# Kernel tuning notes

Hardware: AMD Instinct MI355X
Metric: run time of the kernel (lower is better)

The kernel has to match this reference:

```python
import jax, jax.numpy as jnp
import numpy as np

N, E, G = 20000, 50000, 64          # nodes, edges, graphs
IN_DIM, EDGE_DIM, H, OUT_DIM = 32, 16, 64, 6
EPS = 1e-5  # BatchNorm eps


def setup_inputs() -> dict:
    key = jax.random.key(0)
    ks = jax.random.split(key, 24)
    s = 0.05
    inp = {
        "x": jax.random.normal(ks[0], (N, IN_DIM), jnp.float32),
        "edge_attr": jax.random.normal(ks[1], (E, EDGE_DIM), jnp.float32),
        "src": jax.random.randint(ks[2], (E,), 0, N, jnp.int32),
        "dst": jax.random.randint(ks[3], (E,), 0, N, jnp.int32),
        "batch": jnp.sort(jax.random.randint(ks[4], (N,), 0, G, jnp.int32)),
        # node encoder
        "Wx": jax.random.normal(ks[5], (IN_DIM, H), jnp.float32) * s,
        "bx": jnp.zeros((H,), jnp.float32),
        # three edge MLPs: edge_dim -> H*H
        "We": jax.random.normal(ks[6], (3, EDGE_DIM, H * H), jnp.float32) * s,
        "be": jnp.zeros((3, H * H), jnp.float32),
        # NNConv root weights / biases
        "Wroot": jax.random.normal(ks[7], (3, H, H), jnp.float32) * s,
        "broot": jnp.zeros((3, H), jnp.float32),
        # BatchNorm (eval mode: running stats)
        "gamma": jnp.ones((3, H), jnp.float32),
        "beta": jnp.zeros((3, H), jnp.float32),
        "run_mean": jnp.zeros((3, H), jnp.float32),
        "run_var": jnp.ones((3, H), jnp.float32),
        # head
        "W1": jax.random.normal(ks[8], (H, H), jnp.float32) * s,
        "b1": jnp.zeros((H,), jnp.float32),
        "W2": jax.random.normal(ks[9], (H, OUT_DIM), jnp.float32) * s,
        "b2": jnp.zeros((OUT_DIM,), jnp.float32),
    }
    return inp


def _segment_mean(vals, idx, num_segments):
    tot = jax.ops.segment_sum(vals, idx, num_segments=num_segments)
    cnt = jax.ops.segment_sum(jnp.ones((vals.shape[0],), vals.dtype), idx,
                              num_segments=num_segments)
    return tot / jnp.maximum(cnt, 1.0)[:, None]


def reference(x, edge_attr, src, dst, batch, Wx, bx, We, be, Wroot, broot,
              gamma, beta, run_mean, run_var, W1, b1, W2, b2):
    h = x @ Wx + bx                                      # (N, H)
    for l in range(3):
        # per-edge H x H weight matrices from the edge MLP
        ew = jax.nn.relu(edge_attr @ We[l] + be[l]).reshape(-1, H, H)  # (E, H, H)
        msg = jnp.einsum('eh,eho->eo', h[src], ew)       # gather + per-edge matvec
        agg = _segment_mean(msg, dst, N)                 # scatter-mean at destinations
        out = agg + h @ Wroot[l] + broot[l]              # NNConv root + bias
        out = jax.nn.relu(out)
        # BatchNorm1d in eval mode (running stats); dropout is identity in eval
        out = gamma[l] * (out - run_mean[l]) * jax.lax.rsqrt(run_var[l] + EPS) + beta[l]
        h = out + h                                      # residual (shapes always match)
    pooled = _segment_mean(h, batch, G)                  # global_mean_pool -> (G, H)
    z = jax.nn.relu(pooled @ W1 + b1)
    return z @ W2 + b2                                   # (G, OUT_DIM)
```

## Files before the change

kernel.cpp:

```cpp
#include <hip/hip_runtime.h>
#include <hip/hip_bf16.h>

typedef _Float16 f16x2 __attribute__((ext_vector_type(2)));
typedef _Float16 f16x4 __attribute__((ext_vector_type(4)));
typedef _Float16 f16x8 __attribute__((ext_vector_type(8)));
typedef float    f32x4 __attribute__((ext_vector_type(4)));
typedef float    f32x16 __attribute__((ext_vector_type(16)));

#define IN_DIM   32
#define EDGE_DIM 16
#define HDIM     64
#define OUT_DIM  6
#define BN_EPS   1e-5f

__global__ void k_zero(uint4* __restrict__ p, int n16) {
    int i = blockIdx.x * 256 + threadIdx.x;
    if (i < n16) p[i] = make_uint4(0u, 0u, 0u, 0u);
}

__global__ __launch_bounds__(256) void k_setup(
    const float* __restrict__ We, uint4* __restrict__ WeB,
    const float* __restrict__ x, const float* __restrict__ Wx,
    const float* __restrict__ bx, float* __restrict__ h,
    const float* __restrict__ ea, _Float16* __restrict__ eaH,
    const int* __restrict__ dstI, int* __restrict__ degI,
    const int* __restrict__ batch, int* __restrict__ start,
    int N, int E, int G, int PACKB, int ENCB, int PREPB)
{
    int bid = blockIdx.x;
    int t = threadIdx.x;

    if (bid < PACKB) {
        int tid = bid * 256 + t;
        int tile = tid >> 6, lane = tid & 63;
        int layer = tile >> 7;
        int r = tile & 127;
        int hh = r >> 1, oh = r & 1;
        int col = hh * 64 + oh * 32 + (lane & 31);
        int kbase = 8 * (lane >> 5);
        const float* base = We + (size_t)layer * 65536 + col;
        f16x8 v;
        #pragma unroll
        for (int j = 0; j < 8; ++j) v[j] = (_Float16)base[(size_t)(kbase + j) * 4096];
        WeB[(size_t)tile * 64 + lane] = __builtin_bit_cast(uint4, v);
        return;
    }
    bid -= PACKB;
    if (bid < ENCB) {
        int tid = bid * 256 + t;
        int n = tid >> 4, jq = tid & 15;
        if (n >= N) return;
        const float4* W4 = (const float4*)Wx;
        float4 acc = ((const float4*)bx)[jq];
        const float4* xv = (const float4*)(x + (size_t)n * IN_DIM);
        #pragma unroll
        for (int k4 = 0; k4 < 8; ++k4) {
            float4 xk = xv[k4];
            #pragma unroll
            for (int i = 0; i < 4; ++i) {
                float xs = (i == 0) ? xk.x : (i == 1) ? xk.y : (i == 2) ? xk.z : xk.w;
                float4 ww = W4[(k4 * 4 + i) * 16 + jq];
                acc.x += xs * ww.x; acc.y += xs * ww.y; acc.z += xs * ww.z; acc.w += xs * ww.w;
            }
        }
        ((float4*)h)[tid] = acc;
        return;
    }
    bid -= ENCB;
    if (bid < PREPB) {
        int tid = bid * 256 + t;
        int E8 = E * 8;
        if (tid < E8) {
            float2 v = ((const float2*)ea)[tid];
            f16x2 r; r[0] = (_Float16)v.x; r[1] = (_Float16)v.y;
            ((f16x2*)eaH)[tid] = r;
        }
        if (tid < E) atomicAdd(&degI[dstI[tid]], 1);
        return;
    }
    if (t <= G) {
        int lo = 0, hi = N;
        while (lo < hi) { int mid = (lo + hi) >> 1; if (batch[mid] < t) lo = mid + 1; else hi = mid; }
        start[t] = lo;
    }
}

__global__ void k_scan_local(const int* __restrict__ degI, int* __restrict__ rowptr,
                             int* __restrict__ partials, int N) {
    __shared__ int buf[256];
    int b = blockIdx.x, t = threadIdx.x;
    int i = b * 256 + t;
    int v = (i < N) ? degI[i] : 0;
    buf[t] = v;
    __syncthreads();
    #pragma unroll
    for (int ofs = 1; ofs < 256; ofs <<= 1) {
        int xv = (t >= ofs) ? buf[t - ofs] : 0;
        __syncthreads();
        buf[t] += xv;
        __syncthreads();
    }
    if (i < N) rowptr[i] = buf[t] - v;
    if (t == 255) partials[b] = buf[255];
}

__global__ void k_scan_top(int* __restrict__ partials, int nb) {
    __shared__ int buf[256];
    int t = threadIdx.x;
    int v = (t < nb) ? partials[t] : 0;
    buf[t] = v;
    __syncthreads();
    #pragma unroll
    for (int ofs = 1; ofs < 256; ofs <<= 1) {
        int xv = (t >= ofs) ? buf[t - ofs] : 0;
        __syncthreads();
        buf[t] += xv;
        __syncthreads();
    }
    if (t < nb) partials[t] = buf[t] - v;
    if (t == 0) partials[nb] = buf[255];
}

__global__ void k_scan_add(int* __restrict__ rowptr, int* __restrict__ cursor,
                           const int* __restrict__ partials, int N, int nb) {
    int i = blockIdx.x * 256 + threadIdx.x;
    if (i < N) {
        int r = rowptr[i] + partials[blockIdx.x];
        rowptr[i] = r;
        cursor[i] = r;
    }
    if (i == 0) rowptr[N] = partials[nb];
}

__global__ void k_place(const int* __restrict__ dstI, int* __restrict__ cursor,
                        int* __restrict__ eidx, int E) {
    int e = blockIdx.x * 256 + threadIdx.x;
    if (e < E) {
        int p = atomicAdd(&cursor[dstI[e]], 1);
        eidx[p] = e;
    }
}

__global__ __launch_bounds__(256, 6) void k_edge(
    const uint4* __restrict__ eaH4,
    const uint4* __restrict__ WeB,
    const float* __restrict__ be,
    const float* __restrict__ hin,
    const int* __restrict__ srcI,
    _Float16* __restrict__ msgP,
    int E)
{
    __shared__ float hsT[32][68];
    __shared__ float beL[2048];
    const int t = threadIdx.x;
    const int l = t & 63;
    const int w = t >> 6;
    const int eg = blockIdx.x >> 1;
    const int hhalf = blockIdx.x & 1;
    const int eb = eg * 64;
    const int hbase = hhalf * 32;

    {
        int egc = min(eb + l, E - 1);
        int s = srcI[egc];
        const float4* hp = (const float4*)(hin + (size_t)s * HDIM + hbase + w * 8);
        float4 a = hp[0], b = hp[1];
        hsT[w*8+0][l] = a.x; hsT[w*8+1][l] = a.y; hsT[w*8+2][l] = a.z; hsT[w*8+3][l] = a.w;
        hsT[w*8+4][l] = b.x; hsT[w*8+5][l] = b.y; hsT[w*8+6][l] = b.z; hsT[w*8+7][l] = b.w;
    }
    {
        const float4* bg = (const float4*)(be + hbase * 64);
        float4* bs = (float4*)beL;
        bs[t] = bg[t];
        bs[256 + t] = bg[256 + t];
    }
    __syncthreads();

    const int gp  = w >> 1;
    const int oh  = w & 1;
    const int ebw = eb + gp * 32;
    const int elw = gp * 32;
    const int row = l & 31;
    const int kg  = l >> 5;
    const int obase = oh * 32;

    int ea_e = min(ebw + row, E - 1);
    f16x8 A = __builtin_bit_cast(f16x8, eaH4[(size_t)ea_e * 2 + kg]);

    float m[16];
    #pragma unroll
    for (int j = 0; j < 16; ++j) m[j] = 0.f;

    const uint4* Bb = WeB + (size_t)(hbase * 2 + oh) * 64 + l;
    uint4 Bv = Bb[0];

    for (int hh = 0; hh < 32; ++hh) {
        uint4 Bn;
        if (hh < 31) Bn = Bb[(size_t)(hh + 1) * 128];
        float bias = beL[hh * 64 + obase + (l & 31)];
        f32x16 cin;
        #pragma unroll
        for (int j = 0; j < 16; ++j) cin[j] = bias;
        f32x16 z = __builtin_amdgcn_mfma_f32_32x32x16_f16(
            A, __builtin_bit_cast(f16x8, Bv), cin, 0, 0, 0);
        float4 q0 = *(const float4*)&hsT[hh][elw + 4 * kg + 0];
        float4 q1 = *(const float4*)&hsT[hh][elw + 4 * kg + 8];
        float4 q2 = *(const float4*)&hsT[hh][elw + 4 * kg + 16];
        float4 q3 = *(const float4*)&hsT[hh][elw + 4 * kg + 24];
        m[0]  += fmaxf(z[0],  0.f) * q0.x;
        m[1]  += fmaxf(z[1],  0.f) * q0.y;
        m[2]  += fmaxf(z[2],  0.f) * q0.z;
        m[3]  += fmaxf(z[3],  0.f) * q0.w;
        m[4]  += fmaxf(z[4],  0.f) * q1.x;
        m[5]  += fmaxf(z[5],  0.f) * q1.y;
        m[6]  += fmaxf(z[6],  0.f) * q1.z;
        m[7]  += fmaxf(z[7],  0.f) * q1.w;
        m[8]  += fmaxf(z[8],  0.f) * q2.x;
        m[9]  += fmaxf(z[9],  0.f) * q2.y;
        m[10] += fmaxf(z[10], 0.f) * q2.z;
        m[11] += fmaxf(z[11], 0.f) * q2.w;
        m[12] += fmaxf(z[12], 0.f) * q3.x;
        m[13] += fmaxf(z[13], 0.f) * q3.y;
        m[14] += fmaxf(z[14], 0.f) * q3.z;
        m[15] += fmaxf(z[15], 0.f) * q3.w;
        Bv = Bn;
    }

    _Float16* mw = msgP + (size_t)hhalf * E * 64 + obase + (l & 31);
    #pragma unroll
    for (int j = 0; j < 16; ++j) {
        int e = ebw + (j & 3) + 8 * (j >> 2) + 4 * kg;
        if (e < E) mw[(size_t)e * 64] = (_Float16)m[j];
    }
}

__global__ void k_update(
    const _Float16* __restrict__ msgP, const int* __restrict__ rowptr,
    const int* __restrict__ eidx,
    const float* __restrict__ hin, const float* __restrict__ Wroot,
    const float* __restrict__ broot, const float* __restrict__ gam,
    const float* __restrict__ bet, const float* __restrict__ rmean,
    const float* __restrict__ rvar, float* __restrict__ hout, int N, int E)
{
    int tid = blockIdx.x * 256 + threadIdx.x;
    int n = tid >> 4, jq = tid & 15;
    if (n >= N) return;
    int r0 = rowptr[n], r1 = rowptr[n + 1];
    float4 s = make_float4(0.f, 0.f, 0.f, 0.f);
    const f16x4* m4 = (const f16x4*)msgP;
    for (int i = r0; i < r1; ++i) {
        int eid = eidx[i];
        f16x4 a = m4[(size_t)eid * 16 + jq];
        f16x4 b = m4[((size_t)E + eid) * 16 + jq];
        s.x += (float)a[0] + (float)b[0];
        s.y += (float)a[1] + (float)b[1];
        s.z += (float)a[2] + (float)b[2];
        s.w += (float)a[3] + (float)b[3];
    }
    float dinv = 1.0f / fmaxf((float)(r1 - r0), 1.0f);
    float4 acc = ((const float4*)broot)[jq];
    acc.x += s.x * dinv; acc.y += s.y * dinv; acc.z += s.z * dinv; acc.w += s.w * dinv;
    const float4* W4 = (const float4*)Wroot;
    const float4* hv = (const float4*)(hin + (size_t)n * HDIM);
    #pragma unroll
    for (int k4 = 0; k4 < 16; ++k4) {
        float4 hk = hv[k4];
        #pragma unroll
        for (int i = 0; i < 4; ++i) {
            float hsc = (i == 0) ? hk.x : (i == 1) ? hk.y : (i == 2) ? hk.z : hk.w;
            float4 ww = W4[(k4 * 4 + i) * 16 + jq];
            acc.x += hsc * ww.x; acc.y += hsc * ww.y; acc.z += hsc * ww.z; acc.w += hsc * ww.w;
        }
    }
    acc.x = fmaxf(acc.x, 0.f); acc.y = fmaxf(acc.y, 0.f);
    acc.z = fmaxf(acc.z, 0.f); acc.w = fmaxf(acc.w, 0.f);
    float4 g4 = ((const float4*)gam)[jq];
    float4 b4 = ((const float4*)bet)[jq];
    float4 mm4 = ((const float4*)rmean)[jq];
    float4 v4 = ((const float4*)rvar)[jq];
    float4 hres = ((const float4*)hin)[tid];
    float4 y;
    y.x = g4.x * (acc.x - mm4.x) * rsqrtf(v4.x + BN_EPS) + b4.x + hres.x;
    y.y = g4.y * (acc.y - mm4.y) * rsqrtf(v4.y + BN_EPS) + b4.y + hres.y;
    y.z = g4.z * (acc.z - mm4.z) * rsqrtf(v4.z + BN_EPS) + b4.z + hres.z;
    y.w = g4.w * (acc.w - mm4.w) * rsqrtf(v4.w + BN_EPS) + b4.w + hres.w;
    ((float4*)hout)[tid] = y;
}

__global__ __launch_bounds__(256) void k_pool_head(
    const float* __restrict__ h, const int* __restrict__ start,
    const float* __restrict__ W1, const float* __restrict__ b1,
    const float* __restrict__ W2, const float* __restrict__ b2,
    float* __restrict__ out)
{
    __shared__ float sums[16][68];
    __shared__ float pl[HDIM];
    __shared__ float zl[HDIM];
    int g = blockIdx.x;
    int s0 = start[g], s1 = start[g + 1];
    int t = threadIdx.x, jq = t & 15, rp = t >> 4;
    float4 acc = make_float4(0.f, 0.f, 0.f, 0.f);
    for (int n = s0 + rp; n < s1; n += 16) {
        float4 v = ((const float4*)h)[(size_t)n * 16 + jq];
        acc.x += v.x; acc.y += v.y; acc.z += v.z; acc.w += v.w;
    }
    *(float4*)&sums[rp][jq * 4] = acc;
    __syncthreads();
    if (t < HDIM) {
        float a = 0.f;
        #pragma unroll
        for (int r = 0; r < 16; ++r) a += sums[r][t];
        float cnt = (float)(s1 - s0);
        pl[t] = a / fmaxf(cnt, 1.0f);
    }
    __syncthreads();
    if (t < HDIM) {
        float a = b1[t];
        #pragma unroll
        for (int k = 0; k < HDIM; ++k) a += pl[k] * W1[k * HDIM + t];
        zl[t] = fmaxf(a, 0.f);
    }
    __syncthreads();
    if (t < OUT_DIM) {
        float a = b2[t];
        #pragma unroll
        for (int k = 0; k < HDIM; ++k) a += zl[k] * W2[k * OUT_DIM + t];
        out[(size_t)g * OUT_DIM + t] = a;
    }
}

extern "C" void kernel_launch(void* const* d_in, const int* in_sizes, int n_in,
                              void* d_out, int out_size, void* d_ws, size_t ws_size,
                              hipStream_t stream) {
    const float* x     = (const float*)d_in[0];
    const float* eattr = (const float*)d_in[1];
    const int*   src   = (const int*)d_in[2];
    const int*   dst   = (const int*)d_in[3];
    const int*   batch = (const int*)d_in[4];
    const float* Wx    = (const float*)d_in[5];
    const float* bx    = (const float*)d_in[6];
    const float* We    = (const float*)d_in[7];
    const float* be    = (const float*)d_in[8];
    const float* Wroot = (const float*)d_in[9];
    const float* broot = (const float*)d_in[10];
    const float* gam   = (const float*)d_in[11];
    const float* bet   = (const float*)d_in[12];
    const float* rmean = (const float*)d_in[13];
    const float* rvar  = (const float*)d_in[14];
    const float* W1    = (const float*)d_in[15];
    const float* b1    = (const float*)d_in[16];
    const float* W2    = (const float*)d_in[17];
    const float* b2    = (const float*)d_in[18];
    float* out = (float*)d_out;

    const int N = in_sizes[0] / IN_DIM;
    const int E = in_sizes[2];
    const int G = out_size / OUT_DIM;

    char* ws = (char*)d_ws;
    size_t off = 0;
    auto alloc = [&](size_t bytes) -> void* {
        void* p = ws + off;
        off = (off + bytes + 255) & ~(size_t)255;
        return p;
    };
    float*    h0      = (float*)alloc((size_t)N * HDIM * 4);
    float*    h1      = (float*)alloc((size_t)N * HDIM * 4);
    _Float16* eaH     = (_Float16*)alloc((size_t)E * 16 * 2);
    uint4*    WeB     = (uint4*)alloc((size_t)3 * 128 * 64 * 16);
    int*      start   = (int*)alloc((size_t)(G + 1) * 4);
    int*      rowptr  = (int*)alloc((size_t)(N + 1) * 4);
    int*      cursor  = (int*)alloc((size_t)N * 4);
    int*      eidx    = (int*)alloc((size_t)E * 4);
    _Float16* msgP    = (_Float16*)alloc((size_t)2 * E * HDIM * 2);
    int*      degI    = (int*)alloc((size_t)((N + 3) & ~3) * 4);
    const int nb      = (N + 255) / 256;
    int*      partials= (int*)alloc((size_t)(nb + 1) * 4);
    (void)ws_size; (void)n_in;

    const int n16 = ((N + 3) & ~3) / 4;
    k_zero<<<(n16 + 255) / 256, 256, 0, stream>>>((uint4*)degI, n16);

    const int PACKB = 96;
    const int ENCB  = (N * 16 + 255) / 256;
    const int PREPB = (E * 8 + 255) / 256;
    k_setup<<<PACKB + ENCB + PREPB + 1, 256, 0, stream>>>(
        We, WeB, x, Wx, bx, h0, eattr, eaH, dst, degI, batch, start,
        N, E, G, PACKB, ENCB, PREPB);
    k_scan_local<<<nb, 256, 0, stream>>>(degI, rowptr, partials, N);
    k_scan_top<<<1, 256, 0, stream>>>(partials, nb);
    k_scan_add<<<nb, 256, 0, stream>>>(rowptr, cursor, partials, N, nb);
    k_place<<<(E + 255) / 256, 256, 0, stream>>>(dst, cursor, eidx, E);

    const float* hin = h0;
    float* hout = h1;
    const int edgeBlocks = ((E + 63) / 64) * 2;
    for (int l = 0; l < 3; ++l) {
        k_edge<<<edgeBlocks, 256, 0, stream>>>(
            (const uint4*)eaH, WeB + (size_t)l * 8192, be + (size_t)l * 4096,
            hin, src, msgP, E);
        k_update<<<(N * 16 + 255) / 256, 256, 0, stream>>>(
            msgP, rowptr, eidx, hin, Wroot + (size_t)l * 4096, broot + (size_t)l * 64,
            gam + (size_t)l * 64, bet + (size_t)l * 64, rmean + (size_t)l * 64,
            rvar + (size_t)l * 64, hout, N, E);
        float* tmp = hout; hout = (float*)hin; hin = tmp;
    }
    k_pool_head<<<G, 256, 0, stream>>>(hin, start, W1, b1, W2, b2, out);
}
```

Measured before the change: 195.2 us.

## Fuse whole GNN pipeline into one cooperative kernel with atomic scatter aggregation

Replaces the multi-kernel pipeline (setup, CSR scan/place, per-layer edge and update kernels, pooling) with a single cooperative persistent kernel that uses grid-wide syncs between phases. The CSR build and fp16 message buffer are dropped: edge blocks now cover all 64 input channels and atomically add fp32 messages into a per-node aggregation buffer, which the update phase reads and clears. This removes kernel launch overhead, the scan kernels and a message round-trip through memory. In exchange it adds float atomics contention, grid-sync costs and possibly lower occupancy from the larger shared memory footprint, plus nondeterministic summation order.

```diff
diff --git a/kernel.cpp b/kernel.cpp
--- a/kernel.cpp
+++ b/kernel.cpp
@@ -1,5 +1,8 @@
 #include <hip/hip_runtime.h>
 #include <hip/hip_bf16.h>
+#include <hip/hip_cooperative_groups.h>
+
+namespace cg = cooperative_groups;
 
 typedef _Float16 f16x2 __attribute__((ext_vector_type(2)));
 typedef _Float16 f16x4 __attribute__((ext_vector_type(4)));
@@ -12,6 +15,268 @@
 #define HDIM     64
 #define OUT_DIM  6
 #define BN_EPS   1e-5f
+
+struct FusedParams {
+    const float *x, *ea, *We, *be, *Wx, *bx, *Wroot, *broot, *gam, *bet, *rmean, *rvar, *W1, *b1, *W2, *b2;
+    const int *src, *dst, *batch;
+    float *out;
+    float *h0, *h1, *agg;
+    _Float16 *eaH;
+    uint4 *WeB;
+    int *degI, *start;
+    int N, E, G;
+};
+
+__global__ __launch_bounds__(256, 4) void k_fused(FusedParams p) {
+    cg::grid_group grid = cg::this_grid();
+    __shared__ __align__(16) float hsT[64][68];
+    __shared__ float beL[4096];
+    const int t  = threadIdx.x;
+    const int l  = t & 63;
+    const int w  = t >> 6;
+    const int b0 = blockIdx.x;
+    const int gs = gridDim.x;
+
+    {
+        int nz = p.N * 16;
+        for (int i = b0 * 256 + t; i < nz; i += gs * 256)
+            ((uint4*)p.agg)[i] = make_uint4(0u, 0u, 0u, 0u);
+        for (int i = b0 * 256 + t; i < p.N; i += gs * 256) p.degI[i] = 0;
+    }
+    grid.sync();
+
+    {
+        const int PACKB = 96;
+        const int ENCB  = (p.N * 16 + 255) / 256;
+        const int PREPB = (p.E * 8 + 255) / 256;
+        const int VB    = PACKB + ENCB + PREPB + 1;
+        for (int vb = b0; vb < VB; vb += gs) {
+            if (vb < PACKB) {
+                int tid = vb * 256 + t;
+                int tile = tid >> 6, lane = tid & 63;
+                int layer = tile >> 7;
+                int r = tile & 127;
+                int hh = r >> 1, oh = r & 1;
+                int col = hh * 64 + oh * 32 + (lane & 31);
+                int kbase = 8 * (lane >> 5);
+                const float* base = p.We + (size_t)layer * 65536 + col;
+                f16x8 v;
+                #pragma unroll
+                for (int j = 0; j < 8; ++j) v[j] = (_Float16)base[(size_t)(kbase + j) * 4096];
+                p.WeB[(size_t)tile * 64 + lane] = __builtin_bit_cast(uint4, v);
+            } else if (vb < PACKB + ENCB) {
+                int tid = (vb - PACKB) * 256 + t;
+                int n = tid >> 4, jq = tid & 15;
+                if (n < p.N) {
+                    const float4* W4 = (const float4*)p.Wx;
+                    float4 acc = ((const float4*)p.bx)[jq];
+                    const float4* xv = (const float4*)(p.x + (size_t)n * IN_DIM);
+                    #pragma unroll
+                    for (int k4 = 0; k4 < 8; ++k4) {
+                        float4 xk = xv[k4];
+                        #pragma unroll
+                        for (int i = 0; i < 4; ++i) {
+                            float xs = (i == 0) ? xk.x : (i == 1) ? xk.y : (i == 2) ? xk.z : xk.w;
+                            float4 ww = W4[(k4 * 4 + i) * 16 + jq];
+                            acc.x += xs * ww.x; acc.y += xs * ww.y;
+                            acc.z += xs * ww.z; acc.w += xs * ww.w;
+                        }
+                    }
+                    ((float4*)p.h0)[tid] = acc;
+                }
+            } else if (vb < PACKB + ENCB + PREPB) {
+                int tid = (vb - PACKB - ENCB) * 256 + t;
+                int E8 = p.E * 8;
+                if (tid < E8) {
+                    float2 v = ((const float2*)p.ea)[tid];
+                    f16x2 r2; r2[0] = (_Float16)v.x; r2[1] = (_Float16)v.y;
+                    ((f16x2*)p.eaH)[tid] = r2;
+                }
+                if (tid < p.E) atomicAdd(&p.degI[p.dst[tid]], 1);
+            } else {
+                if (t <= p.G) {
+                    int lo = 0, hi = p.N;
+                    while (lo < hi) { int mid = (lo + hi) >> 1; if (p.batch[mid] < t) lo = mid + 1; else hi = mid; }
+                    p.start[t] = lo;
+                }
+            }
+        }
+    }
+    grid.sync();
+
+    const int EG  = (p.E + 63) / 64;
+    const int NBu = (p.N * 16 + 255) / 256;
+    float* ha = p.h0;
+    float* hb = p.h1;
+
+    #pragma unroll 1
+    for (int layer = 0; layer < 3; ++layer) {
+        const float* hin = ha;
+        float* hout = hb;
+        const uint4* WeL = p.WeB + (size_t)layer * 8192;
+        const float* beG = p.be + (size_t)layer * 4096;
+
+        {
+            const float4* bg = (const float4*)beG;
+            float4* bs = (float4*)beL;
+            for (int i = t; i < 1024; i += 256) bs[i] = bg[i];
+        }
+        __syncthreads();
+
+        const int gp = w >> 1;
+        const int oh = w & 1;
+        const int row = l & 31;
+        const int kg  = l >> 5;
+        const int obase = oh * 32;
+        for (int eg = b0; eg < EG; eg += gs) {
+            const int eb = eg * 64;
+            {
+                int egc = min(eb + l, p.E - 1);
+                int s = p.src[egc];
+                const float4* hp = (const float4*)(hin + (size_t)s * HDIM + w * 16);
+                float4 a = hp[0], b = hp[1], c = hp[2], d = hp[3];
+                hsT[w*16+ 0][l] = a.x; hsT[w*16+ 1][l] = a.y; hsT[w*16+ 2][l] = a.z; hsT[w*16+ 3][l] = a.w;
+                hsT[w*16+ 4][l] = b.x; hsT[w*16+ 5][l] = b.y; hsT[w*16+ 6][l] = b.z; hsT[w*16+ 7][l] = b.w;
+                hsT[w*16+ 8][l] = c.x; hsT[w*16+ 9][l] = c.y; hsT[w*16+10][l] = c.z; hsT[w*16+11][l] = c.w;
+                hsT[w*16+12][l] = d.x; hsT[w*16+13][l] = d.y; hsT[w*16+14][l] = d.z; hsT[w*16+15][l] = d.w;
+            }
+            __syncthreads();
+
+            const int ebw = eb + gp * 32;
+            const int elw = gp * 32;
+            int ea_e = min(ebw + row, p.E - 1);
+            f16x8 A = __builtin_bit_cast(f16x8, ((const uint4*)p.eaH)[(size_t)ea_e * 2 + kg]);
+
+            float m[16];
+            #pragma unroll
+            for (int j = 0; j < 16; ++j) m[j] = 0.f;
+
+            const uint4* Bb = WeL + (size_t)oh * 64 + l;
+            uint4 Bv = Bb[0];
+            for (int hh = 0; hh < 64; ++hh) {
+                uint4 Bn;
+                if (hh < 63) Bn = Bb[(size_t)(hh + 1) * 128];
+                float bias = beL[hh * 64 + obase + row];
+                f32x16 cin;
+                #pragma unroll
+                for (int j = 0; j < 16; ++j) cin[j] = bias;
+                f32x16 z = __builtin_amdgcn_mfma_f32_32x32x16_f16(
+                    A, __builtin_bit_cast(f16x8, Bv), cin, 0, 0, 0);
+                float4 q0 = *(const float4*)&hsT[hh][elw + 4 * kg + 0];
+                float4 q1 = *(const float4*)&hsT[hh][elw + 4 * kg + 8];
+                float4 q2 = *(const float4*)&hsT[hh][elw + 4 * kg + 16];
+                float4 q3 = *(const float4*)&hsT[hh][elw + 4 * kg + 24];
+                m[0]  += fmaxf(z[0],  0.f) * q0.x;
+                m[1]  += fmaxf(z[1],  0.f) * q0.y;
+                m[2]  += fmaxf(z[2],  0.f) * q0.z;
+                m[3]  += fmaxf(z[3],  0.f) * q0.w;
+                m[4]  += fmaxf(z[4],  0.f) * q1.x;
+                m[5]  += fmaxf(z[5],  0.f) * q1.y;
+                m[6]  += fmaxf(z[6],  0.f) * q1.z;
+                m[7]  += fmaxf(z[7],  0.f) * q1.w;
+                m[8]  += fmaxf(z[8],  0.f) * q2.x;
+                m[9]  += fmaxf(z[9],  0.f) * q2.y;
+                m[10] += fmaxf(z[10], 0.f) * q2.z;
+                m[11] += fmaxf(z[11], 0.f) * q2.w;
+                m[12] += fmaxf(z[12], 0.f) * q3.x;
+                m[13] += fmaxf(z[13], 0.f) * q3.y;
+                m[14] += fmaxf(z[14], 0.f) * q3.z;
+                m[15] += fmaxf(z[15], 0.f) * q3.w;
+                Bv = Bn;
+            }
+            #pragma unroll
+            for (int j = 0; j < 16; ++j) {
+                int e = ebw + (j & 3) + 8 * (j >> 2) + 4 * kg;
+                if (e < p.E) {
+                    int d = p.dst[e];
+                    atomicAdd(&p.agg[(size_t)d * HDIM + obase + row], m[j]);
+                }
+            }
+            __syncthreads();
+        }
+        grid.sync();
+
+        for (int vb = b0; vb < NBu; vb += gs) {
+            int tid = vb * 256 + t;
+            int n = tid >> 4, jq = tid & 15;
+            if (n < p.N) {
+                float dinv = 1.0f / fmaxf((float)p.degI[n], 1.0f);
+                float4 acc = ((const float4*)(p.broot + (size_t)layer * 64))[jq];
+                float4 ag = ((const float4*)p.agg)[tid];
+                ((float4*)p.agg)[tid] = make_float4(0.f, 0.f, 0.f, 0.f);
+                acc.x += ag.x * dinv; acc.y += ag.y * dinv;
+                acc.z += ag.z * dinv; acc.w += ag.w * dinv;
+                const float4* W4 = (const float4*)(p.Wroot + (size_t)layer * 4096);
+                const float4* hv = (const float4*)(hin + (size_t)n * HDIM);
+                #pragma unroll
+                for (int k4 = 0; k4 < 16; ++k4) {
+                    float4 hk = hv[k4];
+                    #pragma unroll
+                    for (int i = 0; i < 4; ++i) {
+                        float hsc = (i == 0) ? hk.x : (i == 1) ? hk.y : (i == 2) ? hk.z : hk.w;
+                        float4 ww = W4[(k4 * 4 + i) * 16 + jq];
+                        acc.x += hsc * ww.x; acc.y += hsc * ww.y;
+                        acc.z += hsc * ww.z; acc.w += hsc * ww.w;
+                    }
+                }
+                acc.x = fmaxf(acc.x, 0.f); acc.y = fmaxf(acc.y, 0.f);
+                acc.z = fmaxf(acc.z, 0.f); acc.w = fmaxf(acc.w, 0.f);
+                float4 g4 = ((const float4*)(p.gam + (size_t)layer * 64))[jq];
+                float4 b4 = ((const float4*)(p.bet + (size_t)layer * 64))[jq];
+                float4 mm4 = ((const float4*)(p.rmean + (size_t)layer * 64))[jq];
+                float4 v4 = ((const float4*)(p.rvar + (size_t)layer * 64))[jq];
+                float4 hres = ((const float4*)hin)[tid];
+                float4 y;
+                y.x = g4.x * (acc.x - mm4.x) * rsqrtf(v4.x + BN_EPS) + b4.x + hres.x;
+                y.y = g4.y * (acc.y - mm4.y) * rsqrtf(v4.y + BN_EPS) + b4.y + hres.y;
+                y.z = g4.z * (acc.z - mm4.z) * rsqrtf(v4.z + BN_EPS) + b4.z + hres.z;
+                y.w = g4.w * (acc.w - mm4.w) * rsqrtf(v4.w + BN_EPS) + b4.w + hres.w;
+                ((float4*)hout)[tid] = y;
+            }
+        }
+        grid.sync();
+        float* tmp = hb; hb = ha; ha = tmp;
+    }
+
+    {
+        const float* hf = ha;
+        float* sums = &hsT[0][0];
+        float* pl = beL;
+        float* zl = beL + 64;
+        int jq = t & 15, rp = t >> 4;
+        for (int g = b0; g < p.G; g += gs) {
+            int s0 = p.start[g], s1 = p.start[g + 1];
+            float4 acc = make_float4(0.f, 0.f, 0.f, 0.f);
+            for (int n = s0 + rp; n < s1; n += 16) {
+                float4 v = ((const float4*)hf)[(size_t)n * 16 + jq];
+                acc.x += v.x; acc.y += v.y; acc.z += v.z; acc.w += v.w;
+            }
+            *(float4*)&sums[rp * 68 + jq * 4] = acc;
+            __syncthreads();
+            if (t < HDIM) {
+                float a = 0.f;
+                #pragma unroll
+                for (int r = 0; r < 16; ++r) a += sums[r * 68 + t];
+                pl[t] = a / fmaxf((float)(s1 - s0), 1.0f);
+            }
+            __syncthreads();
+            if (t < HDIM) {
+                float a = p.b1[t];
+                #pragma unroll
+                for (int k = 0; k < HDIM; ++k) a += pl[k] * p.W1[k * HDIM + t];
+                zl[t] = fmaxf(a, 0.f);
+            }
+            __syncthreads();
+            if (t < OUT_DIM) {
+                float a = p.b2[t];
+                #pragma unroll
+                for (int k = 0; k < HDIM; ++k) a += zl[k] * p.W2[k * OUT_DIM + t];
+                p.out[(size_t)g * OUT_DIM + t] = a;
+            }
+            __syncthreads();
+        }
+    }
+}
 
 __global__ void k_zero(uint4* __restrict__ p, int n16) {
     int i = blockIdx.x * 256 + threadIdx.x;
@@ -29,7 +294,6 @@
 {
     int bid = blockIdx.x;
     int t = threadIdx.x;
-
     if (bid < PACKB) {
         int tid = bid * 256 + t;
         int tile = tid >> 6, lane = tid & 63;
@@ -85,181 +349,88 @@
     }
 }
 
-__global__ void k_scan_local(const int* __restrict__ degI, int* __restrict__ rowptr,
-                             int* __restrict__ partials, int N) {
-    __shared__ int buf[256];
-    int b = blockIdx.x, t = threadIdx.x;
-    int i = b * 256 + t;
-    int v = (i < N) ? degI[i] : 0;
-    buf[t] = v;
-    __syncthreads();
-    #pragma unroll
-    for (int ofs = 1; ofs < 256; ofs <<= 1) {
-        int xv = (t >= ofs) ? buf[t - ofs] : 0;
-        __syncthreads();
-        buf[t] += xv;
-        __syncthreads();
-    }
-    if (i < N) rowptr[i] = buf[t] - v;
-    if (t == 255) partials[b] = buf[255];
-}
-
-__global__ void k_scan_top(int* __restrict__ partials, int nb) {
-    __shared__ int buf[256];
-    int t = threadIdx.x;
-    int v = (t < nb) ? partials[t] : 0;
-    buf[t] = v;
-    __syncthreads();
-    #pragma unroll
-    for (int ofs = 1; ofs < 256; ofs <<= 1) {
-        int xv = (t >= ofs) ? buf[t - ofs] : 0;
-        __syncthreads();
-        buf[t] += xv;
-        __syncthreads();
-    }
-    if (t < nb) partials[t] = buf[t] - v;
-    if (t == 0) partials[nb] = buf[255];
-}
-
-__global__ void k_scan_add(int* __restrict__ rowptr, int* __restrict__ cursor,
-                           const int* __restrict__ partials, int N, int nb) {
-    int i = blockIdx.x * 256 + threadIdx.x;
-    if (i < N) {
-        int r = rowptr[i] + partials[blockIdx.x];
-        rowptr[i] = r;
-        cursor[i] = r;
-    }
-    if (i == 0) rowptr[N] = partials[nb];
-}
-
-__global__ void k_place(const int* __restrict__ dstI, int* __restrict__ cursor,
-                        int* __restrict__ eidx, int E) {
-    int e = blockIdx.x * 256 + threadIdx.x;
-    if (e < E) {
-        int p = atomicAdd(&cursor[dstI[e]], 1);
-        eidx[p] = e;
-    }
-}
-
-__global__ __launch_bounds__(256, 6) void k_edge(
-    const uint4* __restrict__ eaH4,
-    const uint4* __restrict__ WeB,
-    const float* __restrict__ be,
-    const float* __restrict__ hin,
-    const int* __restrict__ srcI,
-    _Float16* __restrict__ msgP,
-    int E)
+__global__ __launch_bounds__(256, 4) void k_edge_fb(
+    const uint4* __restrict__ eaH4, const uint4* __restrict__ WeB,
+    const float* __restrict__ be, const float* __restrict__ hin,
+    const int* __restrict__ srcI, const int* __restrict__ dstI,
+    float* __restrict__ agg, int E)
 {
-    __shared__ float hsT[32][68];
-    __shared__ float beL[2048];
+    __shared__ __align__(16) float hsT[64][68];
+    __shared__ float beL[4096];
     const int t = threadIdx.x;
     const int l = t & 63;
     const int w = t >> 6;
-    const int eg = blockIdx.x >> 1;
-    const int hhalf = blockIdx.x & 1;
-    const int eb = eg * 64;
-    const int hbase = hhalf * 32;
-
+    const int eb = blockIdx.x * 64;
+    {
+        const float4* bg = (const float4*)be;
+        float4* bs = (float4*)beL;
+        for (int i = t; i < 1024; i += 256) bs[i] = bg[i];
+    }
     {
         int egc = min(eb + l, E - 1);
         int s = srcI[egc];
-        const float4* hp = (const float4*)(hin + (size_t)s * HDIM + hbase + w * 8);
-        float4 a = hp[0], b = hp[1];
-        hsT[w*8+0][l] = a.x; hsT[w*8+1][l] = a.y; hsT[w*8+2][l] = a.z; hsT[w*8+3][l] = a.w;
-        hsT[w*8+4][l] = b.x; hsT[w*8+5][l] = b.y; hsT[w*8+6][l] = b.z; hsT[w*8+7][l] = b.w;
-    }
-    {
-        const float4* bg = (const float4*)(be + hbase * 64);
-        float4* bs = (float4*)beL;
-        bs[t] = bg[t];
-        bs[256 + t] = bg[256 + t];
+        const float4* hp = (const float4*)(hin + (size_t)s * HDIM + w * 16);
+        float4 a = hp[0], b = hp[1], c = hp[2], d = hp[3];
+        hsT[w*16+ 0][l] = a.x; hsT[w*16+ 1][l] = a.y; hsT[w*16+ 2][l] = a.z; hsT[w*16+ 3][l] = a.w;
+        hsT[w*16+ 4][l] = b.x; hsT[w*16+ 5][l] = b.y; hsT[w*16+ 6][l] = b.z; hsT[w*16+ 7][l] = b.w;
+        hsT[w*16+ 8][l] = c.x; hsT[w*16+ 9][l] = c.y; hsT[w*16+10][l] = c.z; hsT[w*16+11][l] = c.w;
+        hsT[w*16+12][l] = d.x; hsT[w*16+13][l] = d.y; hsT[w*16+14][l] = d.z; hsT[w*16+15][l] = d.w;
     }
     __syncthreads();
-
-    const int gp  = w >> 1;
-    const int oh  = w & 1;
-    const int ebw = eb + gp * 32;
-    const int elw = gp * 32;
-    const int row = l & 31;
-    const int kg  = l >> 5;
-    const int obase = oh * 32;
-
+    const int gp = w >> 1, oh = w & 1;
+    const int ebw = eb + gp * 32, elw = gp * 32;
+    const int row = l & 31, kg = l >> 5, obase = oh * 32;
     int ea_e = min(ebw + row, E - 1);
     f16x8 A = __builtin_bit_cast(f16x8, eaH4[(size_t)ea_e * 2 + kg]);
-
     float m[16];
     #pragma unroll
     for (int j = 0; j < 16; ++j) m[j] = 0.f;
-
-    const uint4* Bb = WeB + (size_t)(hbase * 2 + oh) * 64 + l;
+    const uint4* Bb = WeB + (size_t)oh * 64 + l;
     uint4 Bv = Bb[0];
-
-    for (int hh = 0; hh < 32; ++hh) {
+    for (int hh = 0; hh < 64; ++hh) {
         uint4 Bn;
-        if (hh < 31) Bn = Bb[(size_t)(hh + 1) * 128];
-        float bias = beL[hh * 64 + obase + (l & 31)];
+        if (hh < 63) Bn = Bb[(size_t)(hh + 1) * 128];
+        float bias = beL[hh * 64 + obase + row];
         f32x16 cin;
         #pragma unroll
         for (int j = 0; j < 16; ++j) cin[j] = bias;
-        f32x16 z = __builtin_amdgcn_mfma_f32_32x32x16_f16(
-            A, __builtin_bit_cast(f16x8, Bv), cin, 0, 0, 0);
+        f32x16 z = __builtin_amdgcn_mfma_f32_32x32x16_f16(A, __builtin_bit_cast(f16x8, Bv), cin, 0, 0, 0);
         float4 q0 = *(const float4*)&hsT[hh][elw + 4 * kg + 0];
         float4 q1 = *(const float4*)&hsT[hh][elw + 4 * kg + 8];
         float4 q2 = *(const float4*)&hsT[hh][elw + 4 * kg + 16];
         float4 q3 = *(const float4*)&hsT[hh][elw + 4 * kg + 24];
-        m[0]  += fmaxf(z[0],  0.f) * q0.x;
-        m[1]  += fmaxf(z[1],  0.f) * q0.y;
-        m[2]  += fmaxf(z[2],  0.f) * q0.z;
-        m[3]  += fmaxf(z[3],  0.f) * q0.w;
-        m[4]  += fmaxf(z[4],  0.f) * q1.x;
-        m[5]  += fmaxf(z[5],  0.f) * q1.y;
-        m[6]  += fmaxf(z[6],  0.f) * q1.z;
-        m[7]  += fmaxf(z[7],  0.f) * q1.w;
-        m[8]  += fmaxf(z[8],  0.f) * q2.x;
-        m[9]  += fmaxf(z[9],  0.f) * q2.y;
-        m[10] += fmaxf(z[10], 0.f) * q2.z;
-        m[11] += fmaxf(z[11], 0.f) * q2.w;
-        m[12] += fmaxf(z[12], 0.f) * q3.x;
-        m[13] += fmaxf(z[13], 0.f) * q3.y;
-        m[14] += fmaxf(z[14], 0.f) * q3.z;
-        m[15] += fmaxf(z[15], 0.f) * q3.w;
+        m[0]+=fmaxf(z[0],0.f)*q0.x;  m[1]+=fmaxf(z[1],0.f)*q0.y;
+        m[2]+=fmaxf(z[2],0.f)*q0.z;  m[3]+=fmaxf(z[3],0.f)*q0.w;
+        m[4]+=fmaxf(z[4],0.f)*q1.x;  m[5]+=fmaxf(z[5],0.f)*q1.y;
+        m[6]+=fmaxf(z[6],0.f)*q1.z;  m[7]+=fmaxf(z[7],0.f)*q1.w;
+        m[8]+=fmaxf(z[8],0.f)*q2.x;  m[9]+=fmaxf(z[9],0.f)*q2.y;
+        m[10]+=fmaxf(z[10],0.f)*q2.z; m[11]+=fmaxf(z[11],0.f)*q2.w;
+        m[12]+=fmaxf(z[12],0.f)*q3.x; m[13]+=fmaxf(z[13],0.f)*q3.y;
+        m[14]+=fmaxf(z[14],0.f)*q3.z; m[15]+=fmaxf(z[15],0.f)*q3.w;
         Bv = Bn;
     }
-
-    _Float16* mw = msgP + (size_t)hhalf * E * 64 + obase + (l & 31);
     #pragma unroll
     for (int j = 0; j < 16; ++j) {
         int e = ebw + (j & 3) + 8 * (j >> 2) + 4 * kg;
-        if (e < E) mw[(size_t)e * 64] = (_Float16)m[j];
-    }
-}
-
-__global__ void k_update(
-    const _Float16* __restrict__ msgP, const int* __restrict__ rowptr,
-    const int* __restrict__ eidx,
+        if (e < E) atomicAdd(&agg[(size_t)dstI[e] * HDIM + obase + row], m[j]);
+    }
+}
+
+__global__ void k_update_fb(
+    float* __restrict__ agg, const int* __restrict__ degI,
     const float* __restrict__ hin, const float* __restrict__ Wroot,
     const float* __restrict__ broot, const float* __restrict__ gam,
     const float* __restrict__ bet, const float* __restrict__ rmean,
-    const float* __restrict__ rvar, float* __restrict__ hout, int N, int E)
+    const float* __restrict__ rvar, float* __restrict__ hout, int N)
 {
     int tid = blockIdx.x * 256 + threadIdx.x;
     int n = tid >> 4, jq = tid & 15;
     if (n >= N) return;
-    int r0 = rowptr[n], r1 = rowptr[n + 1];
-    float4 s = make_float4(0.f, 0.f, 0.f, 0.f);
-    const f16x4* m4 = (const f16x4*)msgP;
-    for (int i = r0; i < r1; ++i) {
-        int eid = eidx[i];
-        f16x4 a = m4[(size_t)eid * 16 + jq];
-        f16x4 b = m4[((size_t)E + eid) * 16 + jq];
-        s.x += (float)a[0] + (float)b[0];
-        s.y += (float)a[1] + (float)b[1];
-        s.z += (float)a[2] + (float)b[2];
-        s.w += (float)a[3] + (float)b[3];
-    }
-    float dinv = 1.0f / fmaxf((float)(r1 - r0), 1.0f);
+    float dinv = 1.0f / fmaxf((float)degI[n], 1.0f);
     float4 acc = ((const float4*)broot)[jq];
-    acc.x += s.x * dinv; acc.y += s.y * dinv; acc.z += s.z * dinv; acc.w += s.w * dinv;
+    float4 ag = ((const float4*)agg)[tid];
+    ((float4*)agg)[tid] = make_float4(0.f, 0.f, 0.f, 0.f);
+    acc.x += ag.x * dinv; acc.y += ag.y * dinv; acc.z += ag.z * dinv; acc.w += ag.w * dinv;
     const float4* W4 = (const float4*)Wroot;
     const float4* hv = (const float4*)(hin + (size_t)n * HDIM);
     #pragma unroll
@@ -310,8 +481,7 @@
         float a = 0.f;
         #pragma unroll
         for (int r = 0; r < 16; ++r) a += sums[r][t];
-        float cnt = (float)(s1 - s0);
-        pl[t] = a / fmaxf(cnt, 1.0f);
+        pl[t] = a / fmaxf((float)(s1 - s0), 1.0f);
     }
     __syncthreads();
     if (t < HDIM) {
@@ -364,46 +534,60 @@
         off = (off + bytes + 255) & ~(size_t)255;
         return p;
     };
-    float*    h0      = (float*)alloc((size_t)N * HDIM * 4);
-    float*    h1      = (float*)alloc((size_t)N * HDIM * 4);
-    _Float16* eaH     = (_Float16*)alloc((size_t)E * 16 * 2);
-    uint4*    WeB     = (uint4*)alloc((size_t)3 * 128 * 64 * 16);
-    int*      start   = (int*)alloc((size_t)(G + 1) * 4);
-    int*      rowptr  = (int*)alloc((size_t)(N + 1) * 4);
-    int*      cursor  = (int*)alloc((size_t)N * 4);
-    int*      eidx    = (int*)alloc((size_t)E * 4);
-    _Float16* msgP    = (_Float16*)alloc((size_t)2 * E * HDIM * 2);
-    int*      degI    = (int*)alloc((size_t)((N + 3) & ~3) * 4);
-    const int nb      = (N + 255) / 256;
-    int*      partials= (int*)alloc((size_t)(nb + 1) * 4);
+    float*    h0    = (float*)alloc((size_t)N * HDIM * 4);
+    float*    h1    = (float*)alloc((size_t)N * HDIM * 4);
+    _Float16* eaH   = (_Float16*)alloc((size_t)E * 16 * 2);
+    uint4*    WeB   = (uint4*)alloc((size_t)3 * 128 * 64 * 16);
+    int*      start = (int*)alloc((size_t)(G + 1) * 4);
+    float*    agg   = (float*)alloc((size_t)N * HDIM * 4);
+    int*      degI  = (int*)alloc((size_t)((N + 3) & ~3) * 4);
     (void)ws_size; (void)n_in;
 
-    const int n16 = ((N + 3) & ~3) / 4;
-    k_zero<<<(n16 + 255) / 256, 256, 0, stream>>>((uint4*)degI, n16);
-
-    const int PACKB = 96;
-    const int ENCB  = (N * 16 + 255) / 256;
-    const int PREPB = (E * 8 + 255) / 256;
-    k_setup<<<PACKB + ENCB + PREPB + 1, 256, 0, stream>>>(
-        We, WeB, x, Wx, bx, h0, eattr, eaH, dst, degI, batch, start,
-        N, E, G, PACKB, ENCB, PREPB);
-    k_scan_local<<<nb, 256, 0, stream>>>(degI, rowptr, partials, N);
-    k_scan_top<<<1, 256, 0, stream>>>(partials, nb);
-    k_scan_add<<<nb, 256, 0, stream>>>(rowptr, cursor, partials, N, nb);
-    k_place<<<(E + 255) / 256, 256, 0, stream>>>(dst, cursor, eidx, E);
-
-    const float* hin = h0;
-    float* hout = h1;
-    const int edgeBlocks = ((E + 63) / 64) * 2;
-    for (int l = 0; l < 3; ++l) {
-        k_edge<<<edgeBlocks, 256, 0, stream>>>(
-            (const uint4*)eaH, WeB + (size_t)l * 8192, be + (size_t)l * 4096,
-            hin, src, msgP, E);
-        k_update<<<(N * 16 + 255) / 256, 256, 0, stream>>>(
-            msgP, rowptr, eidx, hin, Wroot + (size_t)l * 4096, broot + (size_t)l * 64,
-            gam + (size_t)l * 64, bet + (size_t)l * 64, rmean + (size_t)l * 64,
-            rvar + (size_t)l * 64, hout, N, E);
-        float* tmp = hout; hout = (float*)hin; hin = tmp;
-    }
-    k_pool_head<<<G, 256, 0, stream>>>(hin, start, W1, b1, W2, b2, out);
-}
+    FusedParams p;
+    p.x = x; p.ea = eattr; p.We = We; p.be = be; p.Wx = Wx; p.bx = bx;
+    p.Wroot = Wroot; p.broot = broot; p.gam = gam; p.bet = bet;
+    p.rmean = rmean; p.rvar = rvar; p.W1 = W1; p.b1 = b1; p.W2 = W2; p.b2 = b2;
+    p.src = src; p.dst = dst; p.batch = batch;
+    p.out = out; p.h0 = h0; p.h1 = h1; p.agg = agg;
+    p.eaH = eaH; p.WeB = WeB; p.degI = degI; p.start = start;
+    p.N = N; p.E = E; p.G = G;
+
+    int maxb = 0;
+    hipError_t qerr = hipOccupancyMaxActiveBlocksPerMultiprocessor(&maxb, k_fused, 256, 0);
+    int grid = 1024;
+    if (qerr == hipSuccess && maxb > 0) {
+        int cap = maxb * 256;
+        if (cap < grid) grid = cap;
+    }
+    if (grid < 1) grid = 256;
+
+    void* args[] = { &p };
+    hipError_t err = hipLaunchCooperativeKernel((const void*)k_fused, dim3(grid), dim3(256),
+                                                args, 0, stream);
+    if (err != hipSuccess) {
+        const int n16 = ((N + 3) & ~3) / 4;
+        const int aggN16 = N * 16;
+        k_zero<<<(aggN16 + 255) / 256, 256, 0, stream>>>((uint4*)agg, aggN16);
+        k_zero<<<(n16 + 255) / 256, 256, 0, stream>>>((uint4*)degI, n16);
+        const int PACKB = 96;
+        const int ENCB  = (N * 16 + 255) / 256;
+        const int PREPB = (E * 8 + 255) / 256;
+        k_setup<<<PACKB + ENCB + PREPB + 1, 256, 0, stream>>>(
+            We, WeB, x, Wx, bx, h0, eattr, eaH, dst, degI, batch, start,
+            N, E, G, PACKB, ENCB, PREPB);
+        const float* hin = h0;
+        float* hout = h1;
+        const int edgeBlocks = (E + 63) / 64;
+        for (int l = 0; l < 3; ++l) {
+            k_edge_fb<<<edgeBlocks, 256, 0, stream>>>(
+                (const uint4*)eaH, WeB + (size_t)l * 8192, be + (size_t)l * 4096,
+                hin, src, dst, agg, E);
+            k_update_fb<<<(N * 16 + 255) / 256, 256, 0, stream>>>(
+                agg, degI, hin, Wroot + (size_t)l * 4096, broot + (size_t)l * 64,
+                gam + (size_t)l * 64, bet + (size_t)l * 64, rmean + (size_t)l * 64,
+                rvar + (size_t)l * 64, hout, N);
+            float* tmp = hout; hout = (float*)hin; hin = tmp;
+        }
+        k_pool_head<<<G, 256, 0, stream>>>(hin, start, W1, b1, W2, b2, out);
+    }
+}
```

New measurement: 766.1 us. +292.4%, slower.

## Scatter edge messages via float atomics instead of CSR gather pipeline

Applied to the files above, without the earlier changes.

Removes the CSR construction kernels (scan, place) and the fp16 per-edge message buffer. The edge kernel now covers all 64 input dims per block and adds each edge's message straight into a float agg buffer at its destination node with atomicAdd. The update kernel reads agg, divides by degree, and zeroes agg for the next layer. This drops four setup launches and the message write-and-read traffic. In exchange it adds atomic contention, makes summation order nondeterministic, doubles shared memory per block, and lowers the occupancy hint.

```diff
diff --git a/kernel.cpp b/kernel.cpp
--- a/kernel.cpp
+++ b/kernel.cpp
@@ -2,9 +2,7 @@
 #include <hip/hip_bf16.h>
 
 typedef _Float16 f16x2 __attribute__((ext_vector_type(2)));
-typedef _Float16 f16x4 __attribute__((ext_vector_type(4)));
 typedef _Float16 f16x8 __attribute__((ext_vector_type(8)));
-typedef float    f32x4 __attribute__((ext_vector_type(4)));
 typedef float    f32x16 __attribute__((ext_vector_type(16)));
 
 #define IN_DIM   32
@@ -29,7 +27,6 @@
 {
     int bid = blockIdx.x;
     int t = threadIdx.x;
-
     if (bid < PACKB) {
         int tid = bid * 256 + t;
         int tile = tid >> 6, lane = tid & 63;
@@ -85,181 +82,88 @@
     }
 }
 
-__global__ void k_scan_local(const int* __restrict__ degI, int* __restrict__ rowptr,
-                             int* __restrict__ partials, int N) {
-    __shared__ int buf[256];
-    int b = blockIdx.x, t = threadIdx.x;
-    int i = b * 256 + t;
-    int v = (i < N) ? degI[i] : 0;
-    buf[t] = v;
-    __syncthreads();
-    #pragma unroll
-    for (int ofs = 1; ofs < 256; ofs <<= 1) {
-        int xv = (t >= ofs) ? buf[t - ofs] : 0;
-        __syncthreads();
-        buf[t] += xv;
-        __syncthreads();
-    }
-    if (i < N) rowptr[i] = buf[t] - v;
-    if (t == 255) partials[b] = buf[255];
-}
-
-__global__ void k_scan_top(int* __restrict__ partials, int nb) {
-    __shared__ int buf[256];
-    int t = threadIdx.x;
-    int v = (t < nb) ? partials[t] : 0;
-    buf[t] = v;
-    __syncthreads();
-    #pragma unroll
-    for (int ofs = 1; ofs < 256; ofs <<= 1) {
-        int xv = (t >= ofs) ? buf[t - ofs] : 0;
-        __syncthreads();
-        buf[t] += xv;
-        __syncthreads();
-    }
-    if (t < nb) partials[t] = buf[t] - v;
-    if (t == 0) partials[nb] = buf[255];
-}
-
-__global__ void k_scan_add(int* __restrict__ rowptr, int* __restrict__ cursor,
-                           const int* __restrict__ partials, int N, int nb) {
-    int i = blockIdx.x * 256 + threadIdx.x;
-    if (i < N) {
-        int r = rowptr[i] + partials[blockIdx.x];
-        rowptr[i] = r;
-        cursor[i] = r;
-    }
-    if (i == 0) rowptr[N] = partials[nb];
-}
-
-__global__ void k_place(const int* __restrict__ dstI, int* __restrict__ cursor,
-                        int* __restrict__ eidx, int E) {
-    int e = blockIdx.x * 256 + threadIdx.x;
-    if (e < E) {
-        int p = atomicAdd(&cursor[dstI[e]], 1);
-        eidx[p] = e;
-    }
-}
-
-__global__ __launch_bounds__(256, 6) void k_edge(
-    const uint4* __restrict__ eaH4,
-    const uint4* __restrict__ WeB,
-    const float* __restrict__ be,
-    const float* __restrict__ hin,
-    const int* __restrict__ srcI,
-    _Float16* __restrict__ msgP,
-    int E)
+__global__ __launch_bounds__(256, 4) void k_edge(
+    const uint4* __restrict__ eaH4, const uint4* __restrict__ WeB,
+    const float* __restrict__ be, const float* __restrict__ hin,
+    const int* __restrict__ srcI, const int* __restrict__ dstI,
+    float* __restrict__ agg, int E)
 {
-    __shared__ float hsT[32][68];
-    __shared__ float beL[2048];
+    __shared__ __align__(16) float hsT[64][68];
+    __shared__ float beL[4096];
     const int t = threadIdx.x;
     const int l = t & 63;
     const int w = t >> 6;
-    const int eg = blockIdx.x >> 1;
-    const int hhalf = blockIdx.x & 1;
-    const int eb = eg * 64;
-    const int hbase = hhalf * 32;
-
+    const int eb = blockIdx.x * 64;
+    {
+        const float4* bg = (const float4*)be;
+        float4* bs = (float4*)beL;
+        for (int i = t; i < 1024; i += 256) bs[i] = bg[i];
+    }
     {
         int egc = min(eb + l, E - 1);
         int s = srcI[egc];
-        const float4* hp = (const float4*)(hin + (size_t)s * HDIM + hbase + w * 8);
-        float4 a = hp[0], b = hp[1];
-        hsT[w*8+0][l] = a.x; hsT[w*8+1][l] = a.y; hsT[w*8+2][l] = a.z; hsT[w*8+3][l] = a.w;
-        hsT[w*8+4][l] = b.x; hsT[w*8+5][l] = b.y; hsT[w*8+6][l] = b.z; hsT[w*8+7][l] = b.w;
-    }
-    {
-        const float4* bg = (const float4*)(be + hbase * 64);
-        float4* bs = (float4*)beL;
-        bs[t] = bg[t];
-        bs[256 + t] = bg[256 + t];
+        const float4* hp = (const float4*)(hin + (size_t)s * HDIM + w * 16);
+        float4 a = hp[0], b = hp[1], c = hp[2], d = hp[3];
+        hsT[w*16+ 0][l] = a.x; hsT[w*16+ 1][l] = a.y; hsT[w*16+ 2][l] = a.z; hsT[w*16+ 3][l] = a.w;
+        hsT[w*16+ 4][l] = b.x; hsT[w*16+ 5][l] = b.y; hsT[w*16+ 6][l] = b.z; hsT[w*16+ 7][l] = b.w;
+        hsT[w*16+ 8][l] = c.x; hsT[w*16+ 9][l] = c.y; hsT[w*16+10][l] = c.z; hsT[w*16+11][l] = c.w;
+        hsT[w*16+12][l] = d.x; hsT[w*16+13][l] = d.y; hsT[w*16+14][l] = d.z; hsT[w*16+15][l] = d.w;
     }
     __syncthreads();
-
-    const int gp  = w >> 1;
-    const int oh  = w & 1;
-    const int ebw = eb + gp * 32;
-    const int elw = gp * 32;
-    const int row = l & 31;
-    const int kg  = l >> 5;
-    const int obase = oh * 32;
-
+    const int gp = w >> 1, oh = w & 1;
+    const int ebw = eb + gp * 32, elw = gp * 32;
+    const int row = l & 31, kg = l >> 5, obase = oh * 32;
     int ea_e = min(ebw + row, E - 1);
     f16x8 A = __builtin_bit_cast(f16x8, eaH4[(size_t)ea_e * 2 + kg]);
-
     float m[16];
     #pragma unroll
     for (int j = 0; j < 16; ++j) m[j] = 0.f;
-
-    const uint4* Bb = WeB + (size_t)(hbase * 2 + oh) * 64 + l;
+    const uint4* Bb = WeB + (size_t)oh * 64 + l;
     uint4 Bv = Bb[0];
-
-    for (int hh = 0; hh < 32; ++hh) {
+    for (int hh = 0; hh < 64; ++hh) {
         uint4 Bn;
-        if (hh < 31) Bn = Bb[(size_t)(hh + 1) * 128];
-        float bias = beL[hh * 64 + obase + (l & 31)];
+        if (hh < 63) Bn = Bb[(size_t)(hh + 1) * 128];
+        float bias = beL[hh * 64 + obase + row];
         f32x16 cin;
         #pragma unroll
         for (int j = 0; j < 16; ++j) cin[j] = bias;
-        f32x16 z = __builtin_amdgcn_mfma_f32_32x32x16_f16(
-            A, __builtin_bit_cast(f16x8, Bv), cin, 0, 0, 0);
+        f32x16 z = __builtin_amdgcn_mfma_f32_32x32x16_f16(A, __builtin_bit_cast(f16x8, Bv), cin, 0, 0, 0);
         float4 q0 = *(const float4*)&hsT[hh][elw + 4 * kg + 0];
         float4 q1 = *(const float4*)&hsT[hh][elw + 4 * kg + 8];
         float4 q2 = *(const float4*)&hsT[hh][elw + 4 * kg + 16];
         float4 q3 = *(const float4*)&hsT[hh][elw + 4 * kg + 24];
-        m[0]  += fmaxf(z[0],  0.f) * q0.x;
-        m[1]  += fmaxf(z[1],  0.f) * q0.y;
-        m[2]  += fmaxf(z[2],  0.f) * q0.z;
-        m[3]  += fmaxf(z[3],  0.f) * q0.w;
-        m[4]  += fmaxf(z[4],  0.f) * q1.x;
-        m[5]  += fmaxf(z[5],  0.f) * q1.y;
-        m[6]  += fmaxf(z[6],  0.f) * q1.z;
-        m[7]  += fmaxf(z[7],  0.f) * q1.w;
-        m[8]  += fmaxf(z[8],  0.f) * q2.x;
-        m[9]  += fmaxf(z[9],  0.f) * q2.y;
-        m[10] += fmaxf(z[10], 0.f) * q2.z;
-        m[11] += fmaxf(z[11], 0.f) * q2.w;
-        m[12] += fmaxf(z[12], 0.f) * q3.x;
-        m[13] += fmaxf(z[13], 0.f) * q3.y;
-        m[14] += fmaxf(z[14], 0.f) * q3.z;
-        m[15] += fmaxf(z[15], 0.f) * q3.w;
+        m[0]+=fmaxf(z[0],0.f)*q0.x;  m[1]+=fmaxf(z[1],0.f)*q0.y;
+        m[2]+=fmaxf(z[2],0.f)*q0.z;  m[3]+=fmaxf(z[3],0.f)*q0.w;
+        m[4]+=fmaxf(z[4],0.f)*q1.x;  m[5]+=fmaxf(z[5],0.f)*q1.y;
+        m[6]+=fmaxf(z[6],0.f)*q1.z;  m[7]+=fmaxf(z[7],0.f)*q1.w;
+        m[8]+=fmaxf(z[8],0.f)*q2.x;  m[9]+=fmaxf(z[9],0.f)*q2.y;
+        m[10]+=fmaxf(z[10],0.f)*q2.z; m[11]+=fmaxf(z[11],0.f)*q2.w;
+        m[12]+=fmaxf(z[12],0.f)*q3.x; m[13]+=fmaxf(z[13],0.f)*q3.y;
+        m[14]+=fmaxf(z[14],0.f)*q3.z; m[15]+=fmaxf(z[15],0.f)*q3.w;
         Bv = Bn;
     }
-
-    _Float16* mw = msgP + (size_t)hhalf * E * 64 + obase + (l & 31);
     #pragma unroll
     for (int j = 0; j < 16; ++j) {
         int e = ebw + (j & 3) + 8 * (j >> 2) + 4 * kg;
-        if (e < E) mw[(size_t)e * 64] = (_Float16)m[j];
+        if (e < E) atomicAdd(&agg[(size_t)dstI[e] * HDIM + obase + row], m[j]);
     }
 }
 
 __global__ void k_update(
-    const _Float16* __restrict__ msgP, const int* __restrict__ rowptr,
-    const int* __restrict__ eidx,
+    float* __restrict__ agg, const int* __restrict__ degI,
     const float* __restrict__ hin, const float* __restrict__ Wroot,
     const float* __restrict__ broot, const float* __restrict__ gam,
     const float* __restrict__ bet, const float* __restrict__ rmean,
-    const float* __restrict__ rvar, float* __restrict__ hout, int N, int E)
+    const float* __restrict__ rvar, float* __restrict__ hout, int N)
 {
     int tid = blockIdx.x * 256 + threadIdx.x;
     int n = tid >> 4, jq = tid & 15;
     if (n >= N) return;
-    int r0 = rowptr[n], r1 = rowptr[n + 1];
-    float4 s = make_float4(0.f, 0.f, 0.f, 0.f);
-    const f16x4* m4 = (const f16x4*)msgP;
-    for (int i = r0; i < r1; ++i) {
-        int eid = eidx[i];
-        f16x4 a = m4[(size_t)eid * 16 + jq];
-        f16x4 b = m4[((size_t)E + eid) * 16 + jq];
-        s.x += (float)a[0] + (float)b[0];
-        s.y += (float)a[1] + (float)b[1];
-        s.z += (float)a[2] + (float)b[2];
-        s.w += (float)a[3] + (float)b[3];
-    }
-    float dinv = 1.0f / fmaxf((float)(r1 - r0), 1.0f);
+    float dinv = 1.0f / fmaxf((float)degI[n], 1.0f);
     float4 acc = ((const float4*)broot)[jq];
-    acc.x += s.x * dinv; acc.y += s.y * dinv; acc.z += s.z * dinv; acc.w += s.w * dinv;
+    float4 ag = ((const float4*)agg)[tid];
+    ((float4*)agg)[tid] = make_float4(0.f, 0.f, 0.f, 0.f);
+    acc.x += ag.x * dinv; acc.y += ag.y * dinv; acc.z += ag.z * dinv; acc.w += ag.w * dinv;
     const float4* W4 = (const float4*)Wroot;
     const float4* hv = (const float4*)(hin + (size_t)n * HDIM);
     #pragma unroll
@@ -310,8 +214,7 @@
         float a = 0.f;
         #pragma unroll
         for (int r = 0; r < 16; ++r) a += sums[r][t];
-        float cnt = (float)(s1 - s0);
-        pl[t] = a / fmaxf(cnt, 1.0f);
+        pl[t] = a / fmaxf((float)(s1 - s0), 1.0f);
     }
     __syncthreads();
     if (t < HDIM) {
@@ -364,22 +267,19 @@
         off = (off + bytes + 255) & ~(size_t)255;
         return p;
     };
-    float*    h0      = (float*)alloc((size_t)N * HDIM * 4);
-    float*    h1      = (float*)alloc((size_t)N * HDIM * 4);
-    _Float16* eaH     = (_Float16*)alloc((size_t)E * 16 * 2);
-    uint4*    WeB     = (uint4*)alloc((size_t)3 * 128 * 64 * 16);
-    int*      start   = (int*)alloc((size_t)(G + 1) * 4);
-    int*      rowptr  = (int*)alloc((size_t)(N + 1) * 4);
-    int*      cursor  = (int*)alloc((size_t)N * 4);
-    int*      eidx    = (int*)alloc((size_t)E * 4);
-    _Float16* msgP    = (_Float16*)alloc((size_t)2 * E * HDIM * 2);
-    int*      degI    = (int*)alloc((size_t)((N + 3) & ~3) * 4);
-    const int nb      = (N + 255) / 256;
-    int*      partials= (int*)alloc((size_t)(nb + 1) * 4);
+    float*    h0    = (float*)alloc((size_t)N * HDIM * 4);
+    float*    h1    = (float*)alloc((size_t)N * HDIM * 4);
+    _Float16* eaH   = (_Float16*)alloc((size_t)E * 16 * 2);
+    uint4*    WeB   = (uint4*)alloc((size_t)3 * 128 * 64 * 16);
+    int*      start = (int*)alloc((size_t)(G + 1) * 4);
+    size_t zoff = off;
+    float*    agg   = (float*)alloc((size_t)N * HDIM * 4);
+    int*      degI  = (int*)alloc((size_t)N * 4);
+    size_t zbytes = off - zoff;
     (void)ws_size; (void)n_in;
 
-    const int n16 = ((N + 3) & ~3) / 4;
-    k_zero<<<(n16 + 255) / 256, 256, 0, stream>>>((uint4*)degI, n16);
+    const int n16 = (int)(zbytes / 16);
+    k_zero<<<(n16 + 255) / 256, 256, 0, stream>>>((uint4*)agg, n16);
 
     const int PACKB = 96;
     const int ENCB  = (N * 16 + 255) / 256;
@@ -387,22 +287,18 @@
     k_setup<<<PACKB + ENCB + PREPB + 1, 256, 0, stream>>>(
         We, WeB, x, Wx, bx, h0, eattr, eaH, dst, degI, batch, start,
         N, E, G, PACKB, ENCB, PREPB);
-    k_scan_local<<<nb, 256, 0, stream>>>(degI, rowptr, partials, N);
-    k_scan_top<<<1, 256, 0, stream>>>(partials, nb);
-    k_scan_add<<<nb, 256, 0, stream>>>(rowptr, cursor, partials, N, nb);
-    k_place<<<(E + 255) / 256, 256, 0, stream>>>(dst, cursor, eidx, E);
 
     const float* hin = h0;
     float* hout = h1;
-    const int edgeBlocks = ((E + 63) / 64) * 2;
+    const int edgeBlocks = (E + 63) / 64;
     for (int l = 0; l < 3; ++l) {
         k_edge<<<edgeBlocks, 256, 0, stream>>>(
             (const uint4*)eaH, WeB + (size_t)l * 8192, be + (size_t)l * 4096,
-            hin, src, msgP, E);
+            hin, src, dst, agg, E);
         k_update<<<(N * 16 + 255) / 256, 256, 0, stream>>>(
-            msgP, rowptr, eidx, hin, Wroot + (size_t)l * 4096, broot + (size_t)l * 64,
+            agg, degI, hin, Wroot + (size_t)l * 4096, broot + (size_t)l * 64,
             gam + (size_t)l * 64, bet + (size_t)l * 64, rmean + (size_t)l * 64,
-            rvar + (size_t)l * 64, hout, N, E);
+            rvar + (size_t)l * 64, hout, N);
         float* tmp = hout; hout = (float*)hin; hin = tmp;
     }
     k_pool_head<<<G, 256, 0, stream>>>(hin, start, W1, b1, W2, b2, out);
```

New measurement: 211.9 us. 8.6% more time.
